# Performance work log

Measured on AMD Instinct MI355X. Metric: run time of the kernel, lower is better.

## Reference

```python
import jax, jax.numpy as jnp
import numpy as np

H = 1024   # hidden_dim
B = 4096   # batch
T = 128    # forecast_len
IN = 1     # output_dim (univariate)


def setup_inputs() -> dict:
    key = jax.random.key(0)
    ks = jax.random.split(key, 8)
    s = 1.0 / np.sqrt(H)  # torch LSTM/Linear default uniform init scale
    u = lambda k, shape: jax.random.uniform(k, shape, jnp.float32, -s, s)
    return {
        "hidden": jax.random.normal(ks[0], (1, B, H), jnp.float32),
        "cell":   jax.random.normal(ks[1], (1, B, H), jnp.float32),
        "W_ih":   u(ks[2], (4 * H, IN)),   # torch gate order: i, f, g, o
        "W_hh":   u(ks[3], (4 * H, H)),
        "b_ih":   u(ks[4], (4 * H,)),
        "b_hh":   u(ks[5], (4 * H,)),
        "W_out":  u(ks[6], (IN, H)),
        "b_out":  u(ks[7], (IN,)),
    }


def reference(hidden, cell, W_ih, W_hh, b_ih, b_hh, W_out, b_out):
    h = hidden[0]  # [B, H]  (num_layers == 1)
    c = cell[0]    # [B, H]
    x0 = jnp.zeros((h.shape[0], IN), h.dtype)  # initial decoder input = zeros
    b = b_ih + b_hh

    def step(carry, _):
        x, h, c = carry
        gates = x @ W_ih.T + h @ W_hh.T + b          # [B, 4H]
        i, f, g, o = jnp.split(gates, 4, axis=-1)    # torch order i,f,g,o
        c = jax.nn.sigmoid(f) * c + jax.nn.sigmoid(i) * jnp.tanh(g)
        h = jax.nn.sigmoid(o) * jnp.tanh(c)
        pred = h @ W_out.T + b_out                   # [B, 1]
        return (pred, h, c), pred                    # prediction fed back as next input

    _, preds = jax.lax.scan(step, (x0, h, c), None, length=T)  # [T, B, 1]
    return jnp.transpose(preds, (1, 0, 2))  # [B, T, 1]
```

## Files before the change

kernel.cpp:

```cpp
#include <hip/hip_runtime.h>
#include <hip/hip_bf16.h>
#include <stdint.h>


#define HH 1024
#define BB 4096
#define TT 128

#define BM 128
#define BJ 32
#define BKK 64

typedef __bf16 bf16;
typedef __bf16 v8bf __attribute__((ext_vector_type(8)));
typedef float f32x4 __attribute__((ext_vector_type(4)));

__device__ __forceinline__ float fast_sigmoid(float x) {
    return 1.0f / (1.0f + __expf(-x));
}
__device__ __forceinline__ float fast_tanh(float x) {
    return 1.0f - 2.0f / (__expf(2.0f * x) + 1.0f);
}

__device__ __forceinline__ void gload_lds16(const void* g, void* l) {
    __builtin_amdgcn_global_load_lds(
        (const __attribute__((address_space(1))) uint32_t*)(uintptr_t)g,
        (__attribute__((address_space(3))) uint32_t*)(uint32_t)(uintptr_t)l,
        16, 0, 0);
}


__global__ void prep_weights(const float* __restrict__ Whh,
                             const float* __restrict__ bih,
                             const float* __restrict__ bhh,
                             bf16* __restrict__ Wr,
                             float* __restrict__ bias) {
    int idx = blockIdx.x * blockDim.x + threadIdx.x;
    if (idx < 4 * HH * HH) {
        int k   = idx & (HH - 1);
        int row = idx >> 10;
        int jb  = row >> 7;
        int g   = (row >> 5) & 3;
        int jj  = row & 31;
        int srow = g * HH + jb * 32 + jj;
        Wr[idx] = (bf16)Whh[srow * HH + k];
    }
    if (idx < 4 * HH) bias[idx] = bih[idx] + bhh[idx];
}

__global__ void prep_h(const float* __restrict__ h0, bf16* __restrict__ hb) {
    int idx = blockIdx.x * blockDim.x + threadIdx.x;
    if (idx < BB * HH) hb[idx] = (bf16)h0[idx];
}

__global__ void prep_pred(float* __restrict__ predbuf, const float* __restrict__ b_out) {
    int idx = blockIdx.x * blockDim.x + threadIdx.x;
    if (idx < (TT + 1) * BB) predbuf[idx] = (idx < BB) ? 0.0f : b_out[0];
}


__global__ __launch_bounds__(256, 4)
void lstm_step(const bf16* __restrict__ hread, bf16* __restrict__ hwrite,
               const float* __restrict__ cin, float* __restrict__ cout,
               const bf16* __restrict__ Wr, const float* __restrict__ bias,
               const float* __restrict__ Wih, const float* __restrict__ Wout,
               const float* __restrict__ predbuf_r, float* __restrict__ predbuf_w) {
    __shared__ bf16 As[BM][BKK];
    __shared__ bf16 Bs[BM][BKK];

    const int tid   = threadIdx.x;
    const int lane  = tid & 63;
    const int w     = tid >> 6;
    const int waveM = w >> 1, waveN = w & 1;
    const int quad  = lane >> 4, l15 = lane & 15;

    const int bid    = blockIdx.x;
    const int jb     = (bid & 7) * 4 + ((bid >> 3) & 3);
    const int blockB = (bid >> 5) * BM;

    f32x4 acc[4][4];
#pragma unroll
    for (int mi = 0; mi < 4; mi++)
#pragma unroll
        for (int g = 0; g < 4; g++) acc[mi][g] = (f32x4){0.f, 0.f, 0.f, 0.f};

    const bf16* Asrc = hread + (size_t)blockB * HH;
    const bf16* Bsrc = Wr + (size_t)jb * 128 * HH;

    const int r8 = lane >> 3;
    const int gc = (lane & 7) ^ r8;
    const int swr = l15 & 7;

    for (int k0 = 0; k0 < HH; k0 += BKK) {
#pragma unroll
        for (int c2 = 0; c2 < 4; c2++) {
            const int rowb = w * 32 + c2 * 8;
            gload_lds16(Asrc + (size_t)(rowb + r8) * HH + k0 + gc * 8, &As[rowb][0]);
            gload_lds16(Bsrc + (size_t)(rowb + r8) * HH + k0 + gc * 8, &Bs[rowb][0]);
        }
        asm volatile("s_waitcnt vmcnt(0)" ::: "memory");
        __syncthreads();
#pragma unroll
        for (int kk = 0; kk < 2; kk++) {
            v8bf a[4], b[4];
            const int pch = ((kk * 4 + quad) ^ swr) * 8;
#pragma unroll
            for (int mi = 0; mi < 4; mi++)
                a[mi] = *(const v8bf*)&As[waveM * 64 + mi * 16 + l15][pch];
#pragma unroll
            for (int g = 0; g < 4; g++)
                b[g] = *(const v8bf*)&Bs[g * 32 + waveN * 16 + l15][pch];
#pragma unroll
            for (int mi = 0; mi < 4; mi++)
#pragma unroll
                for (int g = 0; g < 4; g++)
                    acc[mi][g] = __builtin_amdgcn_mfma_f32_16x16x32_bf16(
                        a[mi], b[g], acc[mi][g], 0, 0, 0);
        }
        __syncthreads();
    }

    const int jj = jb * 32 + waveN * 16 + l15;
    float wih[4], bsv[4];
#pragma unroll
    for (int g = 0; g < 4; g++) {
        wih[g] = Wih[g * HH + jj];
        bsv[g] = bias[g * HH + jj];
    }
    const float wo = Wout[jj];

#pragma unroll
    for (int mi = 0; mi < 4; mi++) {
#pragma unroll
        for (int r = 0; r < 4; r++) {
            const int b = blockB + waveM * 64 + mi * 16 + quad * 4 + r;
            const float x = predbuf_r[b];
            const float gi = acc[mi][0][r] + x * wih[0] + bsv[0];
            const float gf = acc[mi][1][r] + x * wih[1] + bsv[1];
            const float gg = acc[mi][2][r] + x * wih[2] + bsv[2];
            const float go = acc[mi][3][r] + x * wih[3] + bsv[3];
            const float cn = fast_sigmoid(gf) * cin[(size_t)b * HH + jj]
                           + fast_sigmoid(gi) * fast_tanh(gg);
            cout[(size_t)b * HH + jj] = cn;
            const float hn = fast_sigmoid(go) * fast_tanh(cn);
            hwrite[(size_t)b * HH + jj] = (bf16)hn;
            float p = hn * wo;
            p += __shfl_xor(p, 1);
            p += __shfl_xor(p, 2);
            p += __shfl_xor(p, 4);
            p += __shfl_xor(p, 8);
            if (l15 == 0) atomicAdd(&predbuf_w[b], p);
        }
    }
}


__global__ void write_out(const float* __restrict__ predbuf, float* __restrict__ out) {
    int idx = blockIdx.x * blockDim.x + threadIdx.x;
    if (idx < BB * TT) {
        int t = idx & (TT - 1);
        int b = idx >> 7;
        out[idx] = predbuf[(size_t)(t + 1) * BB + b];
    }
}


extern "C" void kernel_launch(void* const* d_in, const int* in_sizes, int n_in,
                              void* d_out, int out_size, void* d_ws, size_t ws_size,
                              hipStream_t stream) {
    const float* hidden = (const float*)d_in[0];
    const float* cell   = (const float*)d_in[1];
    const float* Wih    = (const float*)d_in[2];
    const float* Whh    = (const float*)d_in[3];
    const float* bih    = (const float*)d_in[4];
    const float* bhh    = (const float*)d_in[5];
    const float* Wout   = (const float*)d_in[6];
    const float* bout   = (const float*)d_in[7];
    float* out = (float*)d_out;

    char* ws = (char*)d_ws;
    bf16* Wr = (bf16*)ws;        ws += (size_t)4 * HH * HH * 2;
    bf16* hb0 = (bf16*)ws;       ws += (size_t)BB * HH * 2;
    bf16* hb1 = (bf16*)ws;       ws += (size_t)BB * HH * 2;
    float* cbuf = (float*)ws;    ws += (size_t)BB * HH * 4;
    float* bias = (float*)ws;    ws += (size_t)4 * HH * 4;
    float* predbuf = (float*)ws; ws += (size_t)(TT + 1) * BB * 4;

    prep_weights<<<(4 * HH * HH + 255) / 256, 256, 0, stream>>>(Whh, bih, bhh, Wr, bias);
    prep_h<<<(BB * HH + 255) / 256, 256, 0, stream>>>(hidden, hb0);
    prep_pred<<<((TT + 1) * BB + 255) / 256, 256, 0, stream>>>(predbuf, bout);

    bf16* hb[2] = {hb0, hb1};
    for (int t = 0; t < TT; t++) {
        const bf16* hr = hb[t & 1];
        bf16* hw = hb[(t + 1) & 1];
        const float* ci = (t == 0) ? cell : cbuf;
        lstm_step<<<(HH / BJ) * (BB / BM), 256, 0, stream>>>(
            hr, hw, ci, cbuf, Wr, bias, Wih, Wout,
            predbuf + (size_t)t * BB, predbuf + (size_t)(t + 1) * BB);
    }

    write_out<<<(BB * TT + 255) / 256, 256, 0, stream>>>(predbuf, out);
}
```

Measured before the change: 5.765 ms.

## Use two waves per block with 64x128 per-wave tiles

```diff
diff --git a/kernel.cpp b/kernel.cpp
--- a/kernel.cpp
+++ b/kernel.cpp
@@ -59,7 +59,7 @@
 }
 
 
-__global__ __launch_bounds__(256, 4)
+__global__ __launch_bounds__(128, 2)
 void lstm_step(const bf16* __restrict__ hread, bf16* __restrict__ hwrite,
                const float* __restrict__ cin, float* __restrict__ cout,
                const bf16* __restrict__ Wr, const float* __restrict__ bias,
@@ -68,21 +68,20 @@
     __shared__ bf16 As[BM][BKK];
     __shared__ bf16 Bs[BM][BKK];
 
-    const int tid   = threadIdx.x;
-    const int lane  = tid & 63;
-    const int w     = tid >> 6;
-    const int waveM = w >> 1, waveN = w & 1;
-    const int quad  = lane >> 4, l15 = lane & 15;
+    const int tid  = threadIdx.x;
+    const int lane = tid & 63;
+    const int w    = tid >> 6;
+    const int quad = lane >> 4, l15 = lane & 15;
 
     const int bid    = blockIdx.x;
     const int jb     = (bid & 7) * 4 + ((bid >> 3) & 3);
     const int blockB = (bid >> 5) * BM;
 
-    f32x4 acc[4][4];
+    f32x4 acc[4][8];
 #pragma unroll
     for (int mi = 0; mi < 4; mi++)
 #pragma unroll
-        for (int g = 0; g < 4; g++) acc[mi][g] = (f32x4){0.f, 0.f, 0.f, 0.f};
+        for (int nt = 0; nt < 8; nt++) acc[mi][nt] = (f32x4){0.f, 0.f, 0.f, 0.f};
 
     const bf16* Asrc = hread + (size_t)blockB * HH;
     const bf16* Bsrc = Wr + (size_t)jb * 128 * HH;
@@ -93,8 +92,8 @@
 
     for (int k0 = 0; k0 < HH; k0 += BKK) {
 #pragma unroll
-        for (int c2 = 0; c2 < 4; c2++) {
-            const int rowb = w * 32 + c2 * 8;
+        for (int c2 = 0; c2 < 8; c2++) {
+            const int rowb = w * 64 + c2 * 8;
             gload_lds16(Asrc + (size_t)(rowb + r8) * HH + k0 + gc * 8, &As[rowb][0]);
             gload_lds16(Bsrc + (size_t)(rowb + r8) * HH + k0 + gc * 8, &Bs[rowb][0]);
         }
@@ -102,54 +101,62 @@
         __syncthreads();
 #pragma unroll
         for (int kk = 0; kk < 2; kk++) {
-            v8bf a[4], b[4];
+            v8bf a[4], b[8];
             const int pch = ((kk * 4 + quad) ^ swr) * 8;
 #pragma unroll
             for (int mi = 0; mi < 4; mi++)
-                a[mi] = *(const v8bf*)&As[waveM * 64 + mi * 16 + l15][pch];
-#pragma unroll
-            for (int g = 0; g < 4; g++)
-                b[g] = *(const v8bf*)&Bs[g * 32 + waveN * 16 + l15][pch];
+                a[mi] = *(const v8bf*)&As[w * 64 + mi * 16 + l15][pch];
+#pragma unroll
+            for (int nt = 0; nt < 8; nt++)
+                b[nt] = *(const v8bf*)&Bs[nt * 16 + l15][pch];
 #pragma unroll
             for (int mi = 0; mi < 4; mi++)
 #pragma unroll
-                for (int g = 0; g < 4; g++)
-                    acc[mi][g] = __builtin_amdgcn_mfma_f32_16x16x32_bf16(
-                        a[mi], b[g], acc[mi][g], 0, 0, 0);
+                for (int nt = 0; nt < 8; nt++)
+                    acc[mi][nt] = __builtin_amdgcn_mfma_f32_16x16x32_bf16(
+                        a[mi], b[nt], acc[mi][nt], 0, 0, 0);
         }
         __syncthreads();
     }
 
-    const int jj = jb * 32 + waveN * 16 + l15;
-    float wih[4], bsv[4];
-#pragma unroll
-    for (int g = 0; g < 4; g++) {
-        wih[g] = Wih[g * HH + jj];
-        bsv[g] = bias[g * HH + jj];
-    }
-    const float wo = Wout[jj];
+    float wihv[2][4], bsvv[2][4], wov[2];
+#pragma unroll
+    for (int jh = 0; jh < 2; jh++) {
+        const int j = jb * 32 + jh * 16 + l15;
+#pragma unroll
+        for (int g = 0; g < 4; g++) {
+            wihv[jh][g] = Wih[g * HH + j];
+            bsvv[jh][g] = bias[g * HH + j];
+        }
+        wov[jh] = Wout[j];
+    }
 
 #pragma unroll
     for (int mi = 0; mi < 4; mi++) {
 #pragma unroll
         for (int r = 0; r < 4; r++) {
-            const int b = blockB + waveM * 64 + mi * 16 + quad * 4 + r;
+            const int b = blockB + w * 64 + mi * 16 + quad * 4 + r;
             const float x = predbuf_r[b];
-            const float gi = acc[mi][0][r] + x * wih[0] + bsv[0];
-            const float gf = acc[mi][1][r] + x * wih[1] + bsv[1];
-            const float gg = acc[mi][2][r] + x * wih[2] + bsv[2];
-            const float go = acc[mi][3][r] + x * wih[3] + bsv[3];
-            const float cn = fast_sigmoid(gf) * cin[(size_t)b * HH + jj]
-                           + fast_sigmoid(gi) * fast_tanh(gg);
-            cout[(size_t)b * HH + jj] = cn;
-            const float hn = fast_sigmoid(go) * fast_tanh(cn);
-            hwrite[(size_t)b * HH + jj] = (bf16)hn;
-            float p = hn * wo;
-            p += __shfl_xor(p, 1);
-            p += __shfl_xor(p, 2);
-            p += __shfl_xor(p, 4);
-            p += __shfl_xor(p, 8);
-            if (l15 == 0) atomicAdd(&predbuf_w[b], p);
+            float pacc = 0.0f;
+#pragma unroll
+            for (int jh = 0; jh < 2; jh++) {
+                const int j = jb * 32 + jh * 16 + l15;
+                const float gi = acc[mi][0 + jh][r] + x * wihv[jh][0] + bsvv[jh][0];
+                const float gf = acc[mi][2 + jh][r] + x * wihv[jh][1] + bsvv[jh][1];
+                const float gg = acc[mi][4 + jh][r] + x * wihv[jh][2] + bsvv[jh][2];
+                const float go = acc[mi][6 + jh][r] + x * wihv[jh][3] + bsvv[jh][3];
+                const float cn = fast_sigmoid(gf) * cin[(size_t)b * HH + j]
+                               + fast_sigmoid(gi) * fast_tanh(gg);
+                cout[(size_t)b * HH + j] = cn;
+                const float hn = fast_sigmoid(go) * fast_tanh(cn);
+                hwrite[(size_t)b * HH + j] = (bf16)hn;
+                pacc += hn * wov[jh];
+            }
+            pacc += __shfl_xor(pacc, 1);
+            pacc += __shfl_xor(pacc, 2);
+            pacc += __shfl_xor(pacc, 4);
+            pacc += __shfl_xor(pacc, 8);
+            if (l15 == 0) atomicAdd(&predbuf_w[b], pacc);
         }
     }
 }
@@ -195,7 +202,7 @@
         const bf16* hr = hb[t & 1];
         bf16* hw = hb[(t + 1) & 1];
         const float* ci = (t == 0) ? cell : cbuf;
-        lstm_step<<<(HH / BJ) * (BB / BM), 256, 0, stream>>>(
+        lstm_step<<<(HH / BJ) * (BB / BM), 128, 0, stream>>>(
             hr, hw, ci, cbuf, Wr, bias, Wih, Wout,
             predbuf + (size_t)t * BB, predbuf + (size_t)(t + 1) * BB);
     }
```

Result: slower. 6.132 ms (+6.4%).

## Replace per-step launches with a persistent cooperative kernel using per-batch-block counters

Applied to the files above, without the earlier changes.

```diff
diff --git a/kernel.cpp b/kernel.cpp
--- a/kernel.cpp
+++ b/kernel.cpp
@@ -8,8 +8,8 @@
 #define TT 128
 
 #define BM 128
-#define BJ 32
 #define BKK 64
+#define NTILES 1024
 
 typedef __bf16 bf16;
 typedef __bf16 v8bf __attribute__((ext_vector_type(8)));
@@ -53,18 +53,21 @@
     if (idx < BB * HH) hb[idx] = (bf16)h0[idx];
 }
 
-__global__ void prep_pred(float* __restrict__ predbuf, const float* __restrict__ b_out) {
+__global__ void prep_pred(float* __restrict__ predbuf, const float* __restrict__ b_out,
+                          unsigned* __restrict__ cnt) {
     int idx = blockIdx.x * blockDim.x + threadIdx.x;
     if (idx < (TT + 1) * BB) predbuf[idx] = (idx < BB) ? 0.0f : b_out[0];
+    if (idx < 32 * 16) cnt[idx] = 0u;
 }
 
 
 __global__ __launch_bounds__(256, 4)
-void lstm_step(const bf16* __restrict__ hread, bf16* __restrict__ hwrite,
-               const float* __restrict__ cin, float* __restrict__ cout,
-               const bf16* __restrict__ Wr, const float* __restrict__ bias,
-               const float* __restrict__ Wih, const float* __restrict__ Wout,
-               const float* __restrict__ predbuf_r, float* __restrict__ predbuf_w) {
+void lstm_persist(bf16* __restrict__ hb0, bf16* __restrict__ hb1,
+                  const float* __restrict__ cell0, float* __restrict__ cbuf,
+                  const bf16* __restrict__ Wr, const float* __restrict__ bias,
+                  const float* __restrict__ Wih, const float* __restrict__ Wout,
+                  float* __restrict__ predbuf, unsigned* __restrict__ cnt,
+                  int nblocks) {
     __shared__ bf16 As[BM][BKK];
     __shared__ bf16 Bs[BM][BKK];
 
@@ -74,82 +77,110 @@
     const int waveM = w >> 1, waveN = w & 1;
     const int quad  = lane >> 4, l15 = lane & 15;
 
-    const int bid    = blockIdx.x;
-    const int jb     = (bid & 7) * 4 + ((bid >> 3) & 3);
-    const int blockB = (bid >> 5) * BM;
-
-    f32x4 acc[4][4];
-#pragma unroll
-    for (int mi = 0; mi < 4; mi++)
-#pragma unroll
-        for (int g = 0; g < 4; g++) acc[mi][g] = (f32x4){0.f, 0.f, 0.f, 0.f};
-
-    const bf16* Asrc = hread + (size_t)blockB * HH;
-    const bf16* Bsrc = Wr + (size_t)jb * 128 * HH;
-
-    const int r8 = lane >> 3;
-    const int gc = (lane & 7) ^ r8;
+    const int r8  = lane >> 3;
+    const int gc  = (lane & 7) ^ r8;
     const int swr = l15 & 7;
 
-    for (int k0 = 0; k0 < HH; k0 += BKK) {
-#pragma unroll
-        for (int c2 = 0; c2 < 4; c2++) {
-            const int rowb = w * 32 + c2 * 8;
-            gload_lds16(Asrc + (size_t)(rowb + r8) * HH + k0 + gc * 8, &As[rowb][0]);
-            gload_lds16(Bsrc + (size_t)(rowb + r8) * HH + k0 + gc * 8, &Bs[rowb][0]);
-        }
-        asm volatile("s_waitcnt vmcnt(0)" ::: "memory");
-        __syncthreads();
-#pragma unroll
-        for (int kk = 0; kk < 2; kk++) {
-            v8bf a[4], b[4];
-            const int pch = ((kk * 4 + quad) ^ swr) * 8;
+    for (int t = 0; t < TT; t++) {
+        const bf16* hread = (t & 1) ? hb1 : hb0;
+        bf16*       hwrite = (t & 1) ? hb0 : hb1;
+        const float* cin  = (t == 0) ? cell0 : cbuf;
+        const float* pr   = predbuf + (size_t)t * BB;
+        float*       pw   = predbuf + (size_t)(t + 1) * BB;
+
+        for (int v = blockIdx.x; v < NTILES; v += nblocks) {
+            const int jb     = (v & 7) * 4 + ((v >> 3) & 3);
+            const int bb     = v >> 5;
+            const int blockB = bb * BM;
+            unsigned* arrive = &cnt[bb * 16];
+
+            if (t > 0) {
+                if (tid == 0) {
+                    while (__hip_atomic_load(arrive, __ATOMIC_RELAXED,
+                                             __HIP_MEMORY_SCOPE_AGENT) < 32u * (unsigned)t)
+                        __builtin_amdgcn_s_sleep(2);
+                }
+                __syncthreads();
+                __builtin_amdgcn_fence(__ATOMIC_ACQUIRE, "agent");
+            }
+
+            f32x4 acc[4][4];
 #pragma unroll
             for (int mi = 0; mi < 4; mi++)
-                a[mi] = *(const v8bf*)&As[waveM * 64 + mi * 16 + l15][pch];
-#pragma unroll
-            for (int g = 0; g < 4; g++)
-                b[g] = *(const v8bf*)&Bs[g * 32 + waveN * 16 + l15][pch];
-#pragma unroll
-            for (int mi = 0; mi < 4; mi++)
-#pragma unroll
-                for (int g = 0; g < 4; g++)
-                    acc[mi][g] = __builtin_amdgcn_mfma_f32_16x16x32_bf16(
-                        a[mi], b[g], acc[mi][g], 0, 0, 0);
-        }
-        __syncthreads();
-    }
-
-    const int jj = jb * 32 + waveN * 16 + l15;
-    float wih[4], bsv[4];
-#pragma unroll
-    for (int g = 0; g < 4; g++) {
-        wih[g] = Wih[g * HH + jj];
-        bsv[g] = bias[g * HH + jj];
-    }
-    const float wo = Wout[jj];
-
-#pragma unroll
-    for (int mi = 0; mi < 4; mi++) {
-#pragma unroll
-        for (int r = 0; r < 4; r++) {
-            const int b = blockB + waveM * 64 + mi * 16 + quad * 4 + r;
-            const float x = predbuf_r[b];
-            const float gi = acc[mi][0][r] + x * wih[0] + bsv[0];
-            const float gf = acc[mi][1][r] + x * wih[1] + bsv[1];
-            const float gg = acc[mi][2][r] + x * wih[2] + bsv[2];
-            const float go = acc[mi][3][r] + x * wih[3] + bsv[3];
-            const float cn = fast_sigmoid(gf) * cin[(size_t)b * HH + jj]
-                           + fast_sigmoid(gi) * fast_tanh(gg);
-            cout[(size_t)b * HH + jj] = cn;
-            const float hn = fast_sigmoid(go) * fast_tanh(cn);
-            hwrite[(size_t)b * HH + jj] = (bf16)hn;
-            float p = hn * wo;
-            p += __shfl_xor(p, 1);
-            p += __shfl_xor(p, 2);
-            p += __shfl_xor(p, 4);
-            p += __shfl_xor(p, 8);
-            if (l15 == 0) atomicAdd(&predbuf_w[b], p);
+#pragma unroll
+                for (int g = 0; g < 4; g++) acc[mi][g] = (f32x4){0.f, 0.f, 0.f, 0.f};
+
+            const bf16* Asrc = hread + (size_t)blockB * HH;
+            const bf16* Bsrc = Wr + (size_t)jb * 128 * HH;
+
+            for (int k0 = 0; k0 < HH; k0 += BKK) {
+#pragma unroll
+                for (int c2 = 0; c2 < 4; c2++) {
+                    const int rowb = w * 32 + c2 * 8;
+                    gload_lds16(Asrc + (size_t)(rowb + r8) * HH + k0 + gc * 8, &As[rowb][0]);
+                    gload_lds16(Bsrc + (size_t)(rowb + r8) * HH + k0 + gc * 8, &Bs[rowb][0]);
+                }
+                asm volatile("s_waitcnt vmcnt(0)" ::: "memory");
+                __syncthreads();
+#pragma unroll
+                for (int kk = 0; kk < 2; kk++) {
+                    v8bf a[4], b[4];
+                    const int pch = ((kk * 4 + quad) ^ swr) * 8;
+#pragma unroll
+                    for (int mi = 0; mi < 4; mi++)
+                        a[mi] = *(const v8bf*)&As[waveM * 64 + mi * 16 + l15][pch];
+#pragma unroll
+                    for (int g = 0; g < 4; g++)
+                        b[g] = *(const v8bf*)&Bs[g * 32 + waveN * 16 + l15][pch];
+#pragma unroll
+                    for (int mi = 0; mi < 4; mi++)
+#pragma unroll
+                        for (int g = 0; g < 4; g++)
+                            acc[mi][g] = __builtin_amdgcn_mfma_f32_16x16x32_bf16(
+                                a[mi], b[g], acc[mi][g], 0, 0, 0);
+                }
+                __syncthreads();
+            }
+
+            const int jj = jb * 32 + waveN * 16 + l15;
+            float wih[4], bsv[4];
+#pragma unroll
+            for (int g = 0; g < 4; g++) {
+                wih[g] = Wih[g * HH + jj];
+                bsv[g] = bias[g * HH + jj];
+            }
+            const float wo = Wout[jj];
+
+#pragma unroll
+            for (int mi = 0; mi < 4; mi++) {
+#pragma unroll
+                for (int r = 0; r < 4; r++) {
+                    const int b = blockB + waveM * 64 + mi * 16 + quad * 4 + r;
+                    const float x = pr[b];
+                    const float gi = acc[mi][0][r] + x * wih[0] + bsv[0];
+                    const float gf = acc[mi][1][r] + x * wih[1] + bsv[1];
+                    const float gg = acc[mi][2][r] + x * wih[2] + bsv[2];
+                    const float go = acc[mi][3][r] + x * wih[3] + bsv[3];
+                    const float cn = fast_sigmoid(gf) * cin[(size_t)b * HH + jj]
+                                   + fast_sigmoid(gi) * fast_tanh(gg);
+                    cbuf[(size_t)b * HH + jj] = cn;
+                    const float hn = fast_sigmoid(go) * fast_tanh(cn);
+                    hwrite[(size_t)b * HH + jj] = (bf16)hn;
+                    float p = hn * wo;
+                    p += __shfl_xor(p, 1);
+                    p += __shfl_xor(p, 2);
+                    p += __shfl_xor(p, 4);
+                    p += __shfl_xor(p, 8);
+                    if (l15 == 0) atomicAdd(&pw[b], p);
+                }
+            }
+
+            __syncthreads();
+            if (t + 1 < TT && tid == 0) {
+                __builtin_amdgcn_fence(__ATOMIC_RELEASE, "agent");
+                __hip_atomic_fetch_add(arrive, 1u, __ATOMIC_RELAXED,
+                                       __HIP_MEMORY_SCOPE_AGENT);
+            }
         }
     }
 }
@@ -185,20 +216,25 @@
     float* cbuf = (float*)ws;    ws += (size_t)BB * HH * 4;
     float* bias = (float*)ws;    ws += (size_t)4 * HH * 4;
     float* predbuf = (float*)ws; ws += (size_t)(TT + 1) * BB * 4;
+    unsigned* cnt = (unsigned*)ws; ws += 32 * 16 * 4;
 
     prep_weights<<<(4 * HH * HH + 255) / 256, 256, 0, stream>>>(Whh, bih, bhh, Wr, bias);
     prep_h<<<(BB * HH + 255) / 256, 256, 0, stream>>>(hidden, hb0);
-    prep_pred<<<((TT + 1) * BB + 255) / 256, 256, 0, stream>>>(predbuf, bout);
-
-    bf16* hb[2] = {hb0, hb1};
-    for (int t = 0; t < TT; t++) {
-        const bf16* hr = hb[t & 1];
-        bf16* hw = hb[(t + 1) & 1];
-        const float* ci = (t == 0) ? cell : cbuf;
-        lstm_step<<<(HH / BJ) * (BB / BM), 256, 0, stream>>>(
-            hr, hw, ci, cbuf, Wr, bias, Wih, Wout,
-            predbuf + (size_t)t * BB, predbuf + (size_t)(t + 1) * BB);
-    }
+    prep_pred<<<((TT + 1) * BB + 255) / 256, 256, 0, stream>>>(predbuf, bout, cnt);
+
+    int occ = 0;
+    hipError_t e = hipOccupancyMaxActiveBlocksPerMultiprocessor(&occ, lstm_persist, 256, 0);
+    int nblocks = (e == hipSuccess && occ > 0) ? occ * 256 : 512;
+    if (nblocks > NTILES) nblocks = NTILES;
+
+    const float* cell0 = cell;
+    void* kargs[] = {
+        (void*)&hb0, (void*)&hb1, (void*)&cell0, (void*)&cbuf,
+        (void*)&Wr,  (void*)&bias, (void*)&Wih,  (void*)&Wout,
+        (void*)&predbuf, (void*)&cnt, (void*)&nblocks
+    };
+    hipLaunchCooperativeKernel((const void*)lstm_persist, dim3(nblocks), dim3(256),
+                               kargs, 0, stream);
 
     write_out<<<(BB * TT + 255) / 256, 256, 0, stream>>>(predbuf, out);
 }
```

Result: slower. 13.82 ms (+139.7%).

## Triple-buffer LDS K-tiles with async global-to-LDS prefetch in LSTM step GEMM

Applied to the files above, without the earlier changes.

```diff
diff --git a/kernel.cpp b/kernel.cpp
--- a/kernel.cpp
+++ b/kernel.cpp
@@ -8,8 +8,8 @@
 #define TT 128
 
 #define BM 128
-#define BJ 32
-#define BKK 64
+#define BKK 32
+#define NKT (HH / BKK)
 
 typedef __bf16 bf16;
 typedef __bf16 v8bf __attribute__((ext_vector_type(8)));
@@ -59,14 +59,14 @@
 }
 
 
-__global__ __launch_bounds__(256, 4)
+__global__ __launch_bounds__(256, 3)
 void lstm_step(const bf16* __restrict__ hread, bf16* __restrict__ hwrite,
                const float* __restrict__ cin, float* __restrict__ cout,
                const bf16* __restrict__ Wr, const float* __restrict__ bias,
                const float* __restrict__ Wih, const float* __restrict__ Wout,
                const float* __restrict__ predbuf_r, float* __restrict__ predbuf_w) {
-    __shared__ bf16 As[BM][BKK];
-    __shared__ bf16 Bs[BM][BKK];
+    __shared__ bf16 As[3][BM][BKK];
+    __shared__ bf16 Bs[3][BM][BKK];
 
     const int tid   = threadIdx.x;
     const int lane  = tid & 63;
@@ -87,38 +87,48 @@
     const bf16* Asrc = hread + (size_t)blockB * HH;
     const bf16* Bsrc = Wr + (size_t)jb * 128 * HH;
 
-    const int r8 = lane >> 3;
-    const int gc = (lane & 7) ^ r8;
-    const int swr = l15 & 7;
-
-    for (int k0 = 0; k0 < HH; k0 += BKK) {
-#pragma unroll
-        for (int c2 = 0; c2 < 4; c2++) {
-            const int rowb = w * 32 + c2 * 8;
-            gload_lds16(Asrc + (size_t)(rowb + r8) * HH + k0 + gc * 8, &As[rowb][0]);
-            gload_lds16(Bsrc + (size_t)(rowb + r8) * HH + k0 + gc * 8, &Bs[rowb][0]);
-        }
-        asm volatile("s_waitcnt vmcnt(0)" ::: "memory");
-        __syncthreads();
-#pragma unroll
-        for (int kk = 0; kk < 2; kk++) {
-            v8bf a[4], b[4];
-            const int pch = ((kk * 4 + quad) ^ swr) * 8;
-#pragma unroll
-            for (int mi = 0; mi < 4; mi++)
-                a[mi] = *(const v8bf*)&As[waveM * 64 + mi * 16 + l15][pch];
+    const int r16  = lane >> 2;
+    const int gcol = (((lane & 3) ^ (r16 & 3))) * 8;
+    const int pch  = (quad ^ (l15 & 3)) * 8;
+
+#define STAGE(buf, k0)                                                        \
+    {                                                                         \
+        _Pragma("unroll")                                                     \
+        for (int c2 = 0; c2 < 2; c2++) {                                      \
+            const int rowb = w * 32 + c2 * 16;                                \
+            gload_lds16(Asrc + (size_t)(rowb + r16) * HH + (k0) + gcol,       \
+                        &As[buf][rowb][0]);                                   \
+            gload_lds16(Bsrc + (size_t)(rowb + r16) * HH + (k0) + gcol,       \
+                        &Bs[buf][rowb][0]);                                   \
+        }                                                                     \
+    }
+
+    STAGE(0, 0);
+    STAGE(1, BKK);
+
+#pragma unroll
+    for (int kt = 0; kt < NKT; kt++) {
+        if (kt < NKT - 1) asm volatile("s_waitcnt vmcnt(4)" ::: "memory");
+        else              asm volatile("s_waitcnt vmcnt(0)" ::: "memory");
+        asm volatile("s_barrier" ::: "memory");
+        if (kt + 2 < NKT) STAGE((kt + 2) % 3, (kt + 2) * BKK);
+
+        const int cb = kt % 3;
+        v8bf a[4], b[4];
+#pragma unroll
+        for (int mi = 0; mi < 4; mi++)
+            a[mi] = *(const v8bf*)&As[cb][waveM * 64 + mi * 16 + l15][pch];
+#pragma unroll
+        for (int g = 0; g < 4; g++)
+            b[g] = *(const v8bf*)&Bs[cb][g * 32 + waveN * 16 + l15][pch];
+#pragma unroll
+        for (int mi = 0; mi < 4; mi++)
 #pragma unroll
             for (int g = 0; g < 4; g++)
-                b[g] = *(const v8bf*)&Bs[g * 32 + waveN * 16 + l15][pch];
-#pragma unroll
-            for (int mi = 0; mi < 4; mi++)
-#pragma unroll
-                for (int g = 0; g < 4; g++)
-                    acc[mi][g] = __builtin_amdgcn_mfma_f32_16x16x32_bf16(
-                        a[mi], b[g], acc[mi][g], 0, 0, 0);
-        }
-        __syncthreads();
-    }
+                acc[mi][g] = __builtin_amdgcn_mfma_f32_16x16x32_bf16(
+                    a[mi], b[g], acc[mi][g], 0, 0, 0);
+    }
+#undef STAGE
 
     const int jj = jb * 32 + waveN * 16 + l15;
     float wih[4], bsv[4];
@@ -195,7 +205,7 @@
         const bf16* hr = hb[t & 1];
         bf16* hw = hb[(t + 1) & 1];
         const float* ci = (t == 0) ? cell : cbuf;
-        lstm_step<<<(HH / BJ) * (BB / BM), 256, 0, stream>>>(
+        lstm_step<<<32 * (BB / BM), 256, 0, stream>>>(
             hr, hw, ci, cbuf, Wr, bias, Wih, Wout,
             predbuf + (size_t)t * BB, predbuf + (size_t)(t + 1) * BB);
     }
```

New measurement: 7.250 ms. +25.8%, slower.
